# Performance work log

Hardware: AMD Instinct MI355X
Metric: run time of the kernel (lower is better)

The kernel has to match this reference:

```python
import jax, jax.numpy as jnp
import numpy as np

N = 100000   # nodes
E = 1600000  # edges
F = 64       # node_features


def setup_inputs() -> dict:
    key = jax.random.key(0)
    ks = jax.random.split(key, 8)
    x = jax.random.normal(ks[0], (N, F), dtype=jnp.float32)
    edge_index = jax.random.randint(ks[1], (2, E), 0, N, dtype=jnp.int64)
    edge_weight = jax.random.uniform(ks[2], (E,), dtype=jnp.float32)
    # degrees consistent with the graph (in-degree + 1 to avoid zeros)
    deg = jax.ops.segment_sum(jnp.ones((E,), jnp.float32), edge_index[1], num_segments=N) + 1.0
    W_init = jax.random.normal(ks[3], (F, F), dtype=jnp.float32) / np.sqrt(F)
    gru_wih = jax.random.normal(ks[4], (3 * F, F), dtype=jnp.float32) / np.sqrt(F)
    gru_whh = jax.random.normal(ks[5], (3 * F, F), dtype=jnp.float32) / np.sqrt(F)
    gru_bih = jnp.zeros((3 * F,), jnp.float32)
    gru_bhh = jnp.zeros((3 * F,), jnp.float32)
    lin_w = jax.random.normal(ks[6], (1, F), dtype=jnp.float32) / np.sqrt(F)
    lin_b = jnp.zeros((1,), jnp.float32)
    return {
        "x": x, "edge_index": edge_index, "edge_weight": edge_weight,
        "deg": deg, "target_num": N, "W_init": W_init,
        "gru_wih": gru_wih, "gru_whh": gru_whh,
        "gru_bih": gru_bih, "gru_bhh": gru_bhh,
        "lin_w": lin_w, "lin_b": lin_b,
    }


def _evolve_weight(W, wih, whh, bih, bhh):
    # EvolveGCN-O: GRU with the [F,F] weight matrix as both input and hidden.
    # Rows of W are the "batch"; PyTorch GRU gate order: r, z, n.
    gx = W @ wih.T + bih   # [F, 3F]
    gh = W @ whh.T + bhh   # [F, 3F]
    gx_r, gx_z, gx_n = jnp.split(gx, 3, axis=-1)
    gh_r, gh_z, gh_n = jnp.split(gh, 3, axis=-1)
    r = jax.nn.sigmoid(gx_r + gh_r)
    z = jax.nn.sigmoid(gx_z + gh_z)
    n = jnp.tanh(gx_n + r * gh_n)
    return (1.0 - z) * n + z * W


def reference(x, edge_index, edge_weight, deg, target_num, W_init,
              gru_wih, gru_whh, gru_bih, gru_bhh, lin_w, lin_b):
    # 1) evolve GCN weight with GRU
    W = _evolve_weight(W_init, gru_wih, gru_whh, gru_bih, gru_bhh)
    # 2) GCN conv with fixed evolved W: sym-normalized gather-scatter
    src, dst = edge_index[0], edge_index[1]
    dinv = jax.lax.rsqrt(deg)                       # [N]
    norm = edge_weight * dinv[src] * dinv[dst]      # [E]
    xw = x @ W                                      # [N, F]
    msgs = norm[:, None] * xw[src]                  # [E, F] (irregular gather)
    h = jax.ops.segment_sum(msgs, dst, num_segments=x.shape[0])  # scatter-add
    # 3) keep target nodes, ReLU, linear projection to 1
    h = jax.nn.relu(h[:target_num])
    out = h @ lin_w.T + lin_b                       # [target_num, 1]
    return out
```

## Files before the change

kernel.cpp:

```cpp
#include <hip/hip_runtime.h>
#include <hip/hip_bf16.h>

#define F 64
#define RB 128
#define RBSH 7
#define NBMAX 800
#define CHUNKA 4096
#define CAPR  2816
#define CAPL  3200

typedef int            nt_int4   __attribute__((ext_vector_type(4)));
typedef float          nt_float4 __attribute__((ext_vector_type(4)));

__device__ __forceinline__ unsigned short f2bf(float f) {
    unsigned int u = __float_as_uint(f);
    unsigned int r = (u + 0x7FFFu + ((u >> 16) & 1u)) >> 16;
    return (unsigned short)r;
}
__device__ __forceinline__ unsigned int pack2bf(float lo, float hi) {
    return (unsigned int)f2bf(lo) | ((unsigned int)f2bf(hi) << 16);
}

__global__ void evolve_kernel(const float* __restrict__ W,
                              const float* __restrict__ wih,
                              const float* __restrict__ whh,
                              const float* __restrict__ bih,
                              const float* __restrict__ bhh,
                              float* __restrict__ wt) {
    int t = blockIdx.x * blockDim.x + threadIdx.x;
    if (t >= F * F) return;
    int i = t >> 6;
    int j = t & 63;
    const float* Wi = W + i * F;
    float gxr = bih[j], gxz = bih[F + j], gxn = bih[2 * F + j];
    float ghr = bhh[j], ghz = bhh[F + j], ghn = bhh[2 * F + j];
#pragma unroll
    for (int k = 0; k < F; ++k) {
        float wv = Wi[k];
        gxr += wv * wih[(j) * F + k];
        gxz += wv * wih[(F + j) * F + k];
        gxn += wv * wih[(2 * F + j) * F + k];
        ghr += wv * whh[(j) * F + k];
        ghz += wv * whh[(F + j) * F + k];
        ghn += wv * whh[(2 * F + j) * F + k];
    }
    float r = 1.0f / (1.0f + expf(-(gxr + ghr)));
    float z = 1.0f / (1.0f + expf(-(gxz + ghz)));
    float n = tanhf(gxn + r * ghn);
    float wnew = (1.0f - z) * n + z * Wi[j];
    wt[j * F + i] = wnew;
}

__global__ void __launch_bounds__(256, 1) xw_kernel(
        const float* __restrict__ x,
        const float* __restrict__ wt,
        const float* __restrict__ deg,
        unsigned short* __restrict__ xw16,
        int* __restrict__ gcur, int N, int NB) {
    if (blockIdx.x < 4) {
        int gi = blockIdx.x * 256 + threadIdx.x;
        if (gi < NB) gcur[gi] = gi * CAPR;
    }
    int i = blockIdx.x;
    int rowblk  = (i >> 5) * 8 + (i & 7);
    int quarter = (i >> 3) & 3;
    int r = rowblk * 256 + threadIdx.x;
    if (r >= N) return;
    float xr[F];
    const nt_float4* xp = (const nt_float4*)(x + (size_t)r * F);
#pragma unroll
    for (int q = 0; q < F / 4; ++q) {
        nt_float4 v = xp[q];
        xr[4 * q + 0] = v.x; xr[4 * q + 1] = v.y;
        xr[4 * q + 2] = v.z; xr[4 * q + 3] = v.w;
    }
    float dinv = rsqrtf(deg[r]);
    const float* wbase = wt + quarter * 16 * F;
    unsigned int o[8];
#pragma unroll
    for (int cb = 0; cb < 4; ++cb) {
        const float* w0 = wbase + (4 * cb) * F;
        float a0 = 0.f, a1 = 0.f, a2 = 0.f, a3 = 0.f;
#pragma unroll
        for (int k = 0; k < F; ++k) {
            float xv = xr[k];
            a0 += xv * w0[k];
            a1 += xv * w0[F + k];
            a2 += xv * w0[2 * F + k];
            a3 += xv * w0[3 * F + k];
        }
        o[2 * cb]     = pack2bf(a0 * dinv, a1 * dinv);
        o[2 * cb + 1] = pack2bf(a2 * dinv, a3 * dinv);
    }
    nt_int4* dst = (nt_int4*)(xw16 + (size_t)r * F + quarter * 16);
#pragma unroll
    for (int q = 0; q < 2; ++q) {
        nt_int4 v;
        v.x = (int)o[4 * q + 0]; v.y = (int)o[4 * q + 1];
        v.z = (int)o[4 * q + 2]; v.w = (int)o[4 * q + 3];
        dst[q] = v;
    }
}

__global__ void __launch_bounds__(1024) passA_kernel(
        const int* __restrict__ ei, const float* __restrict__ ew,
        int* __restrict__ gcur,
        unsigned long long* __restrict__ rec, int E, int NB) {
    __shared__ int lh[NBMAX];
    __shared__ int lcur[NBMAX];
    int t = threadIdx.x;
    for (int i = t; i < NB; i += 1024) lh[i] = 0;
    __syncthreads();
    int base = blockIdx.x * CHUNKA;
    int  dstR[4], srcR[4];
    float ewR[4];
    bool ok[4];
#pragma unroll
    for (int it = 0; it < CHUNKA / 1024; ++it) {
        int e = base + it * 1024 + t;
        ok[it] = (e < E);
        if (ok[it]) {
            dstR[it] = ei[E + e];
            srcR[it] = ei[e];
            ewR[it]  = ew[e];
            atomicAdd(&lh[dstR[it] >> RBSH], 1);
        }
    }
    __syncthreads();
    for (int i = t; i < NB; i += 1024) {
        int c = lh[i];
        lcur[i] = c ? atomicAdd(&gcur[i], c) : 0;
    }
    __syncthreads();
#pragma unroll
    for (int it = 0; it < CHUNKA / 1024; ++it) {
        if (ok[it]) {
            unsigned int q = (unsigned int)(ewR[it] * 32767.0f + 0.5f);
            int b = dstR[it] >> RBSH;
            int p = atomicAdd(&lcur[b], 1);
            unsigned long long r = ((unsigned long long)(dstR[it] & (RB - 1)) << 32)
                                 | ((unsigned long long)((unsigned int)srcR[it]) << 15) | q;
            rec[p] = r;
        }
    }
}

__global__ void __launch_bounds__(512) sortsum_kernel(
        const unsigned long long* __restrict__ rec,
        const int* __restrict__ gcur,
        const unsigned short* __restrict__ xw16,
        const float* __restrict__ deg,
        const float* __restrict__ lw,
        const float* __restrict__ lb,
        float* __restrict__ out, int M) {
    __shared__ unsigned int s_rec[CAPL];
    __shared__ int cnt[RB];
    __shared__ int pex[RB];
    __shared__ int cur[RB];
    int b = blockIdx.x;
    int t = threadIdx.x;
    int beg = b * CAPR;
    int end = gcur[b];

    for (int i = t; i < CAPL; i += 512) s_rec[i] = 0u;
    if (t < RB) cnt[t] = 0;
    __syncthreads();

    for (int i = beg + t; i < end; i += 512)
        atomicAdd(&cnt[(int)(rec[i] >> 32)], 1);
    __syncthreads();

    if (t < RB) pex[t] = (cnt[t] + 3) & ~3;
    __syncthreads();
    for (int o = 1; o < RB; o <<= 1) {
        int v = (t < RB && t >= o) ? pex[t - o] : 0;
        __syncthreads();
        if (t < RB) pex[t] += v;
        __syncthreads();
    }
    if (t < RB) {
        int pcnt = (cnt[t] + 3) & ~3;
        int excl = pex[t] - pcnt;
        pex[t] = excl;
        cur[t] = excl;
    }
    __syncthreads();

    for (int i = beg + t; i < end; i += 512) {
        unsigned long long r = rec[i];
        int dl = (int)(r >> 32);
        int p = atomicAdd(&cur[dl], 1);
        s_rec[p] = (unsigned int)r;
    }
    __syncthreads();

    int lane = t & 63;
    int wv = t >> 6;
    int eg = lane >> 4;
    int fq = lane & 15;
    unsigned int flo = (unsigned int)(fq << 3);
    const char* xb = (const char*)xw16;
    float lw0 = lw[4 * fq + 0], lw1 = lw[4 * fq + 1];
    float lw2 = lw[4 * fq + 2], lw3 = lw[4 * fq + 3];
    const float esc = 1.0f / 32767.0f;
    int node0 = b << RBSH;
    for (int nl = wv; nl < RB; nl += 8) {
        int node = node0 + nl;
        if (node >= M) break;
        int nbeg = pex[nl];
        int iters = (cnt[nl] + 3) >> 2;
        float a0 = 0.f, a1 = 0.f, a2 = 0.f, a3 = 0.f;
#pragma unroll 4
        for (int i = 0; i < iters; ++i) {
            unsigned int r = s_rec[nbeg + 4 * i + eg];
            unsigned int off = ((r >> 8) & 0xFFFFFF80u) + flo;
            uint2 u = *(const uint2*)(xb + off);
            float q = (float)(r & 32767u);
            a0 += q * __uint_as_float(u.x << 16);
            a1 += q * __uint_as_float(u.x & 0xFFFF0000u);
            a2 += q * __uint_as_float(u.y << 16);
            a3 += q * __uint_as_float(u.y & 0xFFFF0000u);
        }
        a0 += __shfl_xor(a0, 16, 64); a0 += __shfl_xor(a0, 32, 64);
        a1 += __shfl_xor(a1, 16, 64); a1 += __shfl_xor(a1, 32, 64);
        a2 += __shfl_xor(a2, 16, 64); a2 += __shfl_xor(a2, 32, 64);
        a3 += __shfl_xor(a3, 16, 64); a3 += __shfl_xor(a3, 32, 64);
        float s = fmaxf(a0, 0.f) * lw0 + fmaxf(a1, 0.f) * lw1
                + fmaxf(a2, 0.f) * lw2 + fmaxf(a3, 0.f) * lw3;
#pragma unroll
        for (int o = 8; o; o >>= 1) s += __shfl_xor(s, o, 64);
        if (lane == 0) out[node] = s * (esc * rsqrtf(deg[node])) + lb[0];
    }
}

extern "C" void kernel_launch(void* const* d_in, const int* in_sizes, int n_in,
                              void* d_out, int out_size, void* d_ws, size_t ws_size,
                              hipStream_t stream) {
    const float* x   = (const float*)d_in[0];
    const int*   ei  = (const int*)d_in[1];
    const float* ew  = (const float*)d_in[2];
    const float* deg = (const float*)d_in[3];
    const float* W0  = (const float*)d_in[5];
    const float* wih = (const float*)d_in[6];
    const float* whh = (const float*)d_in[7];
    const float* bih = (const float*)d_in[8];
    const float* bhh = (const float*)d_in[9];
    const float* lw  = (const float*)d_in[10];
    const float* lb  = (const float*)d_in[11];
    float* out = (float*)d_out;

    int N = in_sizes[0] / F;
    int E = in_sizes[1] / 2;
    int M = out_size;
    int NB = (N + RB - 1) / RB;

    float*              wt   = (float*)d_ws;
    unsigned short*     xw16 = (unsigned short*)(wt + 8192);
    unsigned long long* rec  = (unsigned long long*)(xw16 + (size_t)N * F);
    int*                gcur = (int*)(rec + (size_t)NB * CAPR);

    evolve_kernel<<<(F * F + 255) / 256, 256, 0, stream>>>(W0, wih, whh, bih, bhh, wt);

    {
        int nrb8 = (((N + 255) / 256) + 7) & ~7;
        xw_kernel<<<4 * nrb8, 256, 0, stream>>>(x, wt, deg, xw16, gcur, N, NB);
    }

    passA_kernel<<<(E + CHUNKA - 1) / CHUNKA, 1024, 0, stream>>>(ei, ew, gcur, rec, E, NB);

    sortsum_kernel<<<NB, 512, 0, stream>>>(rec, gcur, xw16, deg, lw, lb, out, M);
}
```

Before: 120.5 us.

## Fuse xw projection and edge bucketing into one interleaved kernel launch

Merges the x@W projection kernel and the edge-bucketing pass into a single launch whose blocks alternate between the two roles, so the compute-heavy projection overlaps the memory- and atomic-heavy bucketing. The gcur cursor initialisation moves into the evolve kernel, which now runs before the fused launch. The projection blocks change from 256 to 1024 threads, which raises register pressure (64-float row per thread) under a 1024-thread launch bound and may cause spilling or lower occupancy.

```diff
diff --git a/kernel.cpp b/kernel.cpp
--- a/kernel.cpp
+++ b/kernel.cpp
@@ -26,7 +26,12 @@
                               const float* __restrict__ whh,
                               const float* __restrict__ bih,
                               const float* __restrict__ bhh,
-                              float* __restrict__ wt) {
+                              float* __restrict__ wt,
+                              int* __restrict__ gcur, int NB) {
+    if (blockIdx.x < 4) {
+        int gi = blockIdx.x * 256 + threadIdx.x;
+        if (gi < NB) gcur[gi] = gi * CAPR;
+    }
     int t = blockIdx.x * blockDim.x + threadIdx.x;
     if (t >= F * F) return;
     int i = t >> 6;
@@ -51,96 +56,100 @@
     wt[j * F + i] = wnew;
 }
 
-__global__ void __launch_bounds__(256, 1) xw_kernel(
+__global__ void __launch_bounds__(1024) fused_kernel(
         const float* __restrict__ x,
         const float* __restrict__ wt,
         const float* __restrict__ deg,
         unsigned short* __restrict__ xw16,
-        int* __restrict__ gcur, int N, int NB) {
-    if (blockIdx.x < 4) {
-        int gi = blockIdx.x * 256 + threadIdx.x;
-        if (gi < NB) gcur[gi] = gi * CAPR;
-    }
-    int i = blockIdx.x;
-    int rowblk  = (i >> 5) * 8 + (i & 7);
-    int quarter = (i >> 3) & 3;
-    int r = rowblk * 256 + threadIdx.x;
-    if (r >= N) return;
-    float xr[F];
-    const nt_float4* xp = (const nt_float4*)(x + (size_t)r * F);
-#pragma unroll
-    for (int q = 0; q < F / 4; ++q) {
-        nt_float4 v = xp[q];
-        xr[4 * q + 0] = v.x; xr[4 * q + 1] = v.y;
-        xr[4 * q + 2] = v.z; xr[4 * q + 3] = v.w;
-    }
-    float dinv = rsqrtf(deg[r]);
-    const float* wbase = wt + quarter * 16 * F;
-    unsigned int o[8];
-#pragma unroll
-    for (int cb = 0; cb < 4; ++cb) {
-        const float* w0 = wbase + (4 * cb) * F;
-        float a0 = 0.f, a1 = 0.f, a2 = 0.f, a3 = 0.f;
-#pragma unroll
-        for (int k = 0; k < F; ++k) {
-            float xv = xr[k];
-            a0 += xv * w0[k];
-            a1 += xv * w0[F + k];
-            a2 += xv * w0[2 * F + k];
-            a3 += xv * w0[3 * F + k];
-        }
-        o[2 * cb]     = pack2bf(a0 * dinv, a1 * dinv);
-        o[2 * cb + 1] = pack2bf(a2 * dinv, a3 * dinv);
-    }
-    nt_int4* dst = (nt_int4*)(xw16 + (size_t)r * F + quarter * 16);
-#pragma unroll
-    for (int q = 0; q < 2; ++q) {
-        nt_int4 v;
-        v.x = (int)o[4 * q + 0]; v.y = (int)o[4 * q + 1];
-        v.z = (int)o[4 * q + 2]; v.w = (int)o[4 * q + 3];
-        dst[q] = v;
-    }
-}
-
-__global__ void __launch_bounds__(1024) passA_kernel(
         const int* __restrict__ ei, const float* __restrict__ ew,
         int* __restrict__ gcur,
-        unsigned long long* __restrict__ rec, int E, int NB) {
+        unsigned long long* __restrict__ rec,
+        int N, int E, int NB, int CA, int NXW) {
     __shared__ int lh[NBMAX];
     __shared__ int lcur[NBMAX];
+    int bid = blockIdx.x;
+    bool is_xw;
+    int idx;
+    if (bid < 2 * CA) { is_xw = (bid & 1); idx = bid >> 1; }
+    else              { is_xw = true;      idx = CA + (bid - 2 * CA); }
     int t = threadIdx.x;
-    for (int i = t; i < NB; i += 1024) lh[i] = 0;
-    __syncthreads();
-    int base = blockIdx.x * CHUNKA;
-    int  dstR[4], srcR[4];
-    float ewR[4];
-    bool ok[4];
-#pragma unroll
-    for (int it = 0; it < CHUNKA / 1024; ++it) {
-        int e = base + it * 1024 + t;
-        ok[it] = (e < E);
-        if (ok[it]) {
-            dstR[it] = ei[E + e];
-            srcR[it] = ei[e];
-            ewR[it]  = ew[e];
-            atomicAdd(&lh[dstR[it] >> RBSH], 1);
-        }
-    }
-    __syncthreads();
-    for (int i = t; i < NB; i += 1024) {
-        int c = lh[i];
-        lcur[i] = c ? atomicAdd(&gcur[i], c) : 0;
-    }
-    __syncthreads();
-#pragma unroll
-    for (int it = 0; it < CHUNKA / 1024; ++it) {
-        if (ok[it]) {
-            unsigned int q = (unsigned int)(ewR[it] * 32767.0f + 0.5f);
-            int b = dstR[it] >> RBSH;
-            int p = atomicAdd(&lcur[b], 1);
-            unsigned long long r = ((unsigned long long)(dstR[it] & (RB - 1)) << 32)
-                                 | ((unsigned long long)((unsigned int)srcR[it]) << 15) | q;
-            rec[p] = r;
+
+    if (!is_xw) {
+        for (int i = t; i < NB; i += 1024) lh[i] = 0;
+        __syncthreads();
+        int base = idx * CHUNKA;
+        int  dstR[4], srcR[4];
+        float ewR[4];
+        bool ok[4];
+#pragma unroll
+        for (int it = 0; it < CHUNKA / 1024; ++it) {
+            int e = base + it * 1024 + t;
+            ok[it] = (e < E);
+            if (ok[it]) {
+                dstR[it] = ei[E + e];
+                srcR[it] = ei[e];
+                ewR[it]  = ew[e];
+                atomicAdd(&lh[dstR[it] >> RBSH], 1);
+            }
+        }
+        __syncthreads();
+        for (int i = t; i < NB; i += 1024) {
+            int c = lh[i];
+            lcur[i] = c ? atomicAdd(&gcur[i], c) : 0;
+        }
+        __syncthreads();
+#pragma unroll
+        for (int it = 0; it < CHUNKA / 1024; ++it) {
+            if (ok[it]) {
+                unsigned int q = (unsigned int)(ewR[it] * 32767.0f + 0.5f);
+                int b = dstR[it] >> RBSH;
+                int p = atomicAdd(&lcur[b], 1);
+                unsigned long long r = ((unsigned long long)(dstR[it] & (RB - 1)) << 32)
+                                     | ((unsigned long long)((unsigned int)srcR[it]) << 15) | q;
+                rec[p] = r;
+            }
+        }
+    } else {
+        if (idx >= NXW) return;
+        int a  = idx >> 5;
+        int q4 = (idx >> 3) & 3;
+        int bb = idx & 7;
+        int rowblk = a * 8 + bb;
+        int r = rowblk * 1024 + t;
+        if (r >= N) return;
+        float xr[F];
+        const nt_float4* xp = (const nt_float4*)(x + (size_t)r * F);
+#pragma unroll
+        for (int q = 0; q < F / 4; ++q) {
+            nt_float4 v = xp[q];
+            xr[4 * q + 0] = v.x; xr[4 * q + 1] = v.y;
+            xr[4 * q + 2] = v.z; xr[4 * q + 3] = v.w;
+        }
+        float dinv = rsqrtf(deg[r]);
+        const float* wbase = wt + q4 * 16 * F;
+        unsigned int o[8];
+#pragma unroll
+        for (int cb = 0; cb < 4; ++cb) {
+            const float* w0 = wbase + (4 * cb) * F;
+            float a0 = 0.f, a1 = 0.f, a2 = 0.f, a3 = 0.f;
+#pragma unroll
+            for (int k = 0; k < F; ++k) {
+                float xv = xr[k];
+                a0 += xv * w0[k];
+                a1 += xv * w0[F + k];
+                a2 += xv * w0[2 * F + k];
+                a3 += xv * w0[3 * F + k];
+            }
+            o[2 * cb]     = pack2bf(a0 * dinv, a1 * dinv);
+            o[2 * cb + 1] = pack2bf(a2 * dinv, a3 * dinv);
+        }
+        nt_int4* dst = (nt_int4*)(xw16 + (size_t)r * F + q4 * 16);
+#pragma unroll
+        for (int q = 0; q < 2; ++q) {
+            nt_int4 v;
+            v.x = (int)o[4 * q + 0]; v.y = (int)o[4 * q + 1];
+            v.z = (int)o[4 * q + 2]; v.w = (int)o[4 * q + 3];
+            dst[q] = v;
         }
     }
 }
@@ -259,14 +268,17 @@
     unsigned long long* rec  = (unsigned long long*)(xw16 + (size_t)N * F);
     int*                gcur = (int*)(rec + (size_t)NB * CAPR);
 
-    evolve_kernel<<<(F * F + 255) / 256, 256, 0, stream>>>(W0, wih, whh, bih, bhh, wt);
+    evolve_kernel<<<(F * F + 255) / 256, 256, 0, stream>>>(W0, wih, whh, bih, bhh, wt, gcur, NB);
 
     {
-        int nrb8 = (((N + 255) / 256) + 7) & ~7;
-        xw_kernel<<<4 * nrb8, 256, 0, stream>>>(x, wt, deg, xw16, gcur, N, NB);
-    }
-
-    passA_kernel<<<(E + CHUNKA - 1) / CHUNKA, 1024, 0, stream>>>(ei, ew, gcur, rec, E, NB);
+        int CA   = (E + CHUNKA - 1) / CHUNKA;
+        int nrb  = (N + 1023) / 1024;
+        int nrb8 = (nrb + 7) & ~7;
+        int NXW  = 4 * nrb8;
+        int grid = 2 * CA + (NXW > CA ? NXW - CA : 0);
+        fused_kernel<<<grid, 1024, 0, stream>>>(x, wt, deg, xw16, ei, ew,
+                                                gcur, rec, N, E, NB, CA, NXW);
+    }
 
     sortsum_kernel<<<NB, 512, 0, stream>>>(rec, gcur, xw16, deg, lw, lb, out, M);
 }
```

Result: slower. 133.5 us (+10.8%).
